# Kernel optimization log

Measured on AMD Instinct MI355X. Metric: run time of the kernel, lower is better.

## Reference

```python
import jax, jax.numpy as jnp
import numpy as np

K = 16
EPS = 1e-5
SLOPE = 0.2


def knn_idx(k, xyz_k, xyz_q):
    # xyz_k: (B,Nk,3), xyz_q: (B,Nq,3) -> (B,Nq,k) indices of k nearest in xyz_k
    d = (jnp.sum(xyz_q * xyz_q, -1, keepdims=True)
         - 2.0 * jnp.einsum('bqc,bkc->bqk', xyz_q, xyz_k)
         + jnp.sum(xyz_k * xyz_k, -1)[:, None, :])
    _, idx = jax.lax.top_k(-d, k)
    return idx


def graph_feature(coor_q, x_q, coor_k, x_k):
    # coor_*: (B,N*,3); x_q: (B,C,Nq); x_k: (B,C,Nk) -> (B,2C,Nq,K)
    idx = knn_idx(K, coor_k, coor_q)                      # (B,Nq,K)
    nbr = jax.vmap(lambda xk, i: xk[:, i])(x_k, idx)       # (B,C,Nq,K)
    xq = x_q[:, :, :, None]                                # (B,C,Nq,1)
    xq = jnp.broadcast_to(xq, nbr.shape)
    return jnp.concatenate([nbr - xq, xq], axis=1)


def group_norm(x, gamma, beta, groups=4):
    B, C, N, Kk = x.shape
    xg = x.reshape(B, groups, C // groups, N, Kk)
    mu = jnp.mean(xg, axis=(2, 3, 4), keepdims=True)
    var = jnp.var(xg, axis=(2, 3, 4), keepdims=True)
    xn = ((xg - mu) / jnp.sqrt(var + EPS)).reshape(B, C, N, Kk)
    return xn * gamma[None, :, None, None] + beta[None, :, None, None]


def cgl(f, W, gamma, beta):
    # 1x1 Conv2d (no bias) + GroupNorm(4) + LeakyReLU(0.2)
    y = jnp.einsum('oc,bcnk->bonk', W, f)
    return jax.nn.leaky_relu(group_norm(y, gamma, beta), SLOPE)


def fps(xyz, m):
    # furthest point sampling. xyz: (B,N,3) -> (B,m) int32
    B, N, _ = xyz.shape
    first = jnp.zeros((B,), jnp.int32)

    def body(carry, _):
        dist, last = carry
        lp = jnp.take_along_axis(xyz, last[:, None, None].astype(jnp.int32), axis=1)  # (B,1,3)
        d = jnp.sum((xyz - lp) ** 2, -1)
        dist = jnp.minimum(dist, d)
        nxt = jnp.argmax(dist, -1).astype(jnp.int32)
        return (dist, nxt), nxt

    init = (jnp.full((B, N), 1e10, jnp.float32), first)
    _, rest = jax.lax.scan(body, init, None, length=m - 1)  # (m-1,B)
    return jnp.concatenate([first[None, :], rest], axis=0).T  # (B,m)


def fps_downsample(coor, x, m):
    # coor: (B,N,3), x: (B,C,N) -> new_coor (B,3,m), new_x (B,C,m)
    idx = fps(coor, m)                                        # (B,m)
    new_coor = jnp.take_along_axis(coor, idx[:, :, None], axis=1).transpose(0, 2, 1)
    new_x = jnp.take_along_axis(x, idx[:, None, :], axis=2)
    return new_coor, new_x


def setup_inputs() -> dict:
    key = jax.random.key(0)
    ks = jax.random.split(key, 16)
    d = {
        'x': jax.random.normal(ks[0], (8, 4096, 3), jnp.float32),
        'num0': 2048, 'num1': 512, 'num2': 128,
        'w_in': jax.random.normal(ks[1], (8, 3), jnp.float32) * 0.3,
        'b_in': jnp.zeros((8,), jnp.float32),
    }
    layer_dims = {'1': (32, 16), '2': (64, 64), '4': (128, 128),
                  '5': (128, 256), '6': (256, 256), '7': (256, 512)}
    for i, (name, (o, c)) in enumerate(layer_dims.items()):
        d[f'w{name}'] = jax.random.normal(ks[2 + i], (o, c), jnp.float32) * (1.0 / np.sqrt(c))
        d[f'g{name}'] = jnp.ones((o,), jnp.float32)
        d[f'be{name}'] = jnp.zeros((o,), jnp.float32)
    return d


def reference(x, num0, num1, num2, w_in, b_in,
              w1, g1, be1, w2, g2, be2, w4, g4, be4,
              w5, g5, be5, w6, g6, be6, w7, g7, be7):
    xyz = x.transpose(0, 2, 1)                                # (B,3,N)
    coor = x                                                  # (B,N,3)
    f = jnp.einsum('oc,bcn->bon', w_in, xyz) + b_in[None, :, None]  # (B,8,N)

    f = cgl(graph_feature(coor, f, coor, f), w1, g1, be1)     # (B,32,N,K)
    f = jnp.max(f, axis=-1)                                   # (B,32,N)

    sp1, f_q = fps_downsample(coor, f, num0)                  # (B,3,n0),(B,32,n0)
    coor_d = sp1.transpose(0, 2, 1)                           # (B,n0,3)
    f = cgl(graph_feature(coor_d, f_q, coor, f), w2, g2, be2)
    stage1_feature = jnp.max(f, axis=-1)                      # (B,64,n0)
    coor = coor_d

    sp2, f_q = fps_downsample(coor, stage1_feature, num1)
    coor_d = sp2.transpose(0, 2, 1)
    f = cgl(graph_feature(coor_d, f_q, coor, stage1_feature), w4, g4, be4)
    f = jnp.max(f, axis=-1)                                   # (B,128,n1)
    f = cgl(graph_feature(coor_d, f, coor_d, f), w5, g5, be5)
    stage2_feature = jnp.max(f, axis=-1)                      # (B,128,n1)
    coor = coor_d

    sp3, f_q = fps_downsample(coor, stage2_feature, num2)
    coor_d = sp3.transpose(0, 2, 1)
    f = cgl(graph_feature(coor_d, f_q, coor, stage2_feature), w6, g6, be6)
    f = jnp.max(f, axis=-1)                                   # (B,256,n2)
    f = cgl(graph_feature(coor_d, f, coor_d, f), w7, g7, be7)
    stage3_feature = jnp.max(f, axis=-1)                      # (B,256,n2)

    out_coor = sp3.transpose(0, 2, 1)                         # (B,n2,3)
    out_f = stage3_feature.transpose(0, 2, 1)                 # (B,n2,256)
    return out_coor, out_f
```

## Files before the change

kernel.cpp:

```cpp
#include <hip/hip_runtime.h>
#include <hip/hip_bf16.h>
#include <math.h>

#define DEVI __device__ __forceinline__
typedef unsigned long long ull;
typedef float f32x2 __attribute__((ext_vector_type(2)));

__global__ void k_feat0(const float* __restrict__ x,
                        const float* __restrict__ w_in,
                        const float* __restrict__ b_in,
                        float* __restrict__ coords0, float* __restrict__ feat0,
                        float* __restrict__ stats)
{
  int t = blockIdx.x*blockDim.x + threadIdx.x;
  if (t < 384) stats[t] = 0.f;
  if (t >= 8*4096) return;
  float cx = x[t*3+0], cy = x[t*3+1], cz = x[t*3+2];
  coords0[t*3+0]=cx; coords0[t*3+1]=cy; coords0[t*3+2]=cz;
  #pragma unroll
  for (int o=0;o<8;o++){
    float s = __fadd_rn(__fadd_rn(__fmul_rn(cx,w_in[o*3+0]),
                                  __fmul_rn(cy,w_in[o*3+1])),
                        __fmul_rn(cz,w_in[o*3+2]));
    feat0[t*8+o] = __fadd_rn(s, b_in[o]);
  }
}

DEVI f32x2 pk_sub(f32x2 a, f32x2 b){
  f32x2 r;
  asm("v_pk_add_f32 %0, %1, %2 neg_lo:[0,1] neg_hi:[0,1]" : "=v"(r) : "v"(a), "v"(b));
  return r;
}
DEVI f32x2 pk_mul(f32x2 a, f32x2 b){
  f32x2 r; asm("v_pk_mul_f32 %0, %1, %2" : "=v"(r) : "v"(a), "v"(b)); return r;
}
DEVI f32x2 pk_add(f32x2 a, f32x2 b){
  f32x2 r; asm("v_pk_add_f32 %0, %1, %2" : "=v"(r) : "v"(a), "v"(b)); return r;
}

template<int CTRL>
DEVI float dppmaxf(float x){
  float o = __int_as_float(__builtin_amdgcn_update_dpp(__float_as_int(x),__float_as_int(x),CTRL,0xF,0xF,false));
  return fmaxf(x,o);
}
template<int CTRL>
DEVI unsigned dppminu(unsigned x){
  unsigned o = (unsigned)__builtin_amdgcn_update_dpp((int)x,(int)x,CTRL,0xF,0xF,false);
  return (x < o) ? x : o;
}

template<int P>
DEVI void fps_stage(f32x2 (&px)[P/2], f32x2 (&py)[P/2], f32x2 (&pz)[P/2],
                    int m, float sx, float sy, float sz,
                    const float* cpx, const float* cpy, const float* cpz,
                    ull* mK,
                    int* ssel, float* snx, float* sny, float* snz, int tid)
{
  const int wv = tid>>6, lane = tid&63;
  float dist[P];
  #pragma unroll
  for (int p=0;p<P;p++) dist[p]=1e10f;
  if (tid==0){ ssel[0]=0; if (snx){ snx[0]=sx; sny[0]=sy; snz[0]=sz; } }
  #pragma unroll 1
  for (int it=1; it<m; it++){
    f32x2 vsx, vsy, vsz;
    vsx.x=sx; vsx.y=sx; vsy.x=sy; vsy.y=sy; vsz.x=sz; vsz.y=sz;
    float bv = -1.f;
    #pragma unroll
    for (int i=0;i<P/2;i++){
      f32x2 dx = pk_sub(px[i], vsx);
      f32x2 dy = pk_sub(py[i], vsy);
      f32x2 dz = pk_sub(pz[i], vsz);
      f32x2 s  = pk_add(pk_add(pk_mul(dx,dx), pk_mul(dy,dy)), pk_mul(dz,dz));
      float d0 = fminf(dist[2*i],   s.x);
      float d1 = fminf(dist[2*i+1], s.y);
      dist[2*i] = d0; dist[2*i+1] = d1;
      bv = fmaxf(bv, d0);
      bv = fmaxf(bv, d1);
    }
    int bidx = 0;
    #pragma unroll
    for (int p=P-1;p>=0;p--) if (dist[p]==bv) bidx = tid+(p<<8);
    float w = bv;
    w = dppmaxf<0x111>(w);
    w = dppmaxf<0x112>(w);
    w = dppmaxf<0x114>(w);
    w = dppmaxf<0x118>(w);
    w = dppmaxf<0x142>(w);
    w = dppmaxf<0x143>(w);
    float bvw = __uint_as_float((unsigned)__builtin_amdgcn_readlane(__float_as_int(w),63));
    unsigned cand = (bv == bvw) ? (unsigned)bidx : 0xFFFFFFFFu;
    cand = dppminu<0x111>(cand);
    cand = dppminu<0x112>(cand);
    cand = dppminu<0x114>(cand);
    cand = dppminu<0x118>(cand);
    cand = dppminu<0x142>(cand);
    cand = dppminu<0x143>(cand);
    const unsigned itu = (unsigned)it;
    ull* slot = mK + ((it&1)<<2);
    if (lane==63){
      unsigned lo = ((~cand & 0xFFFu)<<12) | itu;
      *(volatile ull*)(slot + wv) = ((ull)__float_as_uint(bvw)<<32) | (ull)lo;
    }
    ull k0,k1,k2,k3;
    for (;;){
      asm volatile("" ::: "memory");
      k0=slot[0]; k1=slot[1]; k2=slot[2]; k3=slot[3];
      unsigned chk = (((unsigned)k0 ^ itu) | ((unsigned)k1 ^ itu) |
                      ((unsigned)k2 ^ itu) | ((unsigned)k3 ^ itu)) & 0xFFFu;
      if (chk == 0u) break;
    }
    ull ka = (k1>k0)?k1:k0;
    ull kb = (k3>k2)?k3:k2;
    ull kw = (kb>ka)?kb:ka;
    int gi = (int)((~((unsigned)(kw & 0xffffffffull) >> 12)) & 0xFFFu);
    sx = cpx[gi]; sy = cpy[gi]; sz = cpz[gi];
    if (tid==0){
      ssel[it]=gi;
      if (snx){ snx[it]=sx; sny[it]=sy; snz[it]=sz; }
    }
  }
}

template<int CTRL>
DEVI void dppmin_fj(float& d, int& j){
  float od = __int_as_float(__builtin_amdgcn_update_dpp(__float_as_int(d),__float_as_int(d),CTRL,0xF,0xF,false));
  int   oj = __builtin_amdgcn_update_dpp(j,j,CTRL,0xF,0xF,false);
  bool tk = (od < d) || (od == d && oj < j);
  d = tk?od:d; j = tk?oj:j;
}

DEVI float dist_qk(const float* __restrict__ ckb, int j,
                   float qx, float qy, float qz, float sqq){
  float kx=ckb[3*j], ky=ckb[3*j+1], kz=ckb[3*j+2];
  float sk  = __fadd_rn(__fadd_rn(__fmul_rn(kx,kx),__fmul_rn(ky,ky)),
                        __fmul_rn(kz,kz));
  float dot = __fadd_rn(__fadd_rn(__fmul_rn(qx,kx),__fmul_rn(qy,ky)),
                        __fmul_rn(qz,kz));
  return __fadd_rn(__fsub_rn(sqq, __fmul_rn(2.0f,dot)), sk);
}

template<int NPL>
DEVI void knn_wave(const float* __restrict__ cq, int Nq,
                   const float* __restrict__ ck, int Nk,
                   int* __restrict__ idx_out, int b, int q, int lane)
{
  size_t r3 = ((size_t)b*Nq+q)*3;
  float qx=cq[r3], qy=cq[r3+1], qz=cq[r3+2];
  float sqq = __fadd_rn(__fadd_rn(__fmul_rn(qx,qx),__fmul_rn(qy,qy)),
                        __fmul_rn(qz,qz));
  constexpr int GS = (NPL < 8) ? NPL : 8;
  constexpr int NG = NPL / GS;
  float gv[NG]; int gj[NG];
  const float* ckb = ck + (size_t)b*Nk*3;
  ull exmask = 0;
  int dirtyg = -1;
  int myout = 0;
  #pragma unroll 1
  for (int r=0; r<16; r++){
    #pragma unroll
    for (int g=0; g<NG; g++){
      if (dirtyg < 0 || dirtyg == g){
        float nv=__int_as_float(0x7f800000); int nj=0x7fffffff;
        #pragma unroll
        for (int e=0; e<GS; e++){
          const int i = g*GS+e;
          int j = lane + (i<<6);
          float d = dist_qk(ckb, j, qx,qy,qz, sqq);
          bool rem = ((exmask >> i) & 1ull) == 0ull;
          if (rem && d < nv){ nv=d; nj=j; }
        }
        gv[g]=nv; gj[g]=nj;
      }
    }
    float lv = gv[0]; int lj = gj[0];
    #pragma unroll
    for (int g=1; g<NG; g++)
      if (gv[g]<lv || (gv[g]==lv && gj[g]<lj)){ lv=gv[g]; lj=gj[g]; }
    float rd = lv; int rj = lj;
    dppmin_fj<0x111>(rd,rj);
    dppmin_fj<0x112>(rd,rj);
    dppmin_fj<0x114>(rd,rj);
    dppmin_fj<0x118>(rd,rj);
    dppmin_fj<0x142>(rd,rj);
    dppmin_fj<0x143>(rd,rj);
    int wj = __builtin_amdgcn_readlane(rj,63);
    if (lane == r) myout = wj;
    if ((wj & 63) == lane) exmask |= (1ull << (wj>>6));
    dirtyg = (wj>>6)/GS;
  }
  if (lane<16) idx_out[((size_t)b*Nq+q)*16 + lane] = myout;
}

__global__ __launch_bounds__(256) void k_fps_knn1(
    const float* __restrict__ coords0,
    int* __restrict__ idx1, int* __restrict__ idx2, int* __restrict__ idx3,
    float* __restrict__ c1, float* __restrict__ c2, float* __restrict__ c3,
    float* __restrict__ out, int* __restrict__ knn1)
{
  __shared__ float s1x[4096], s1y[4096], s1z[4096];
  __shared__ float s2x[2048], s2y[2048], s2z[2048];
  __shared__ float s3x[512],  s3y[512],  s3z[512];
  __shared__ float s4x[128],  s4y[128],  s4z[128];
  __shared__ int   ssel[2048];
  __shared__ alignas(32) ull mK[8];
  if (blockIdx.x >= 8){
    int flat = blockIdx.x - 8;
    int b = flat >> 10, qb = flat & 1023;
    int q = qb*4 + (threadIdx.x>>6);
    knn_wave<64>(coords0, 4096, coords0, 4096, knn1, b, q, threadIdx.x&63);
    return;
  }
  const int b = blockIdx.x, tid = threadIdx.x;
  __builtin_amdgcn_s_setprio(3);
  const float* cb = coords0 + (size_t)b*4096*3;
  if (tid<8) mK[tid] = ~0ull;
  {
    f32x2 px[8], py[8], pz[8];
    #pragma unroll
    for (int i=0;i<8;i++){
      int j0 = tid + ((2*i)<<8), j1 = tid + ((2*i+1)<<8);
      float X0=cb[3*j0], Y0=cb[3*j0+1], Z0=cb[3*j0+2];
      float X1=cb[3*j1], Y1=cb[3*j1+1], Z1=cb[3*j1+2];
      px[i].x=X0; px[i].y=X1; py[i].x=Y0; py[i].y=Y1; pz[i].x=Z0; pz[i].y=Z1;
      s1x[j0]=X0; s1y[j0]=Y0; s1z[j0]=Z0;
      s1x[j1]=X1; s1y[j1]=Y1; s1z[j1]=Z1;
    }
    float sx=cb[0], sy=cb[1], sz=cb[2];
    __syncthreads();
    fps_stage<16>(px,py,pz, 2048, sx,sy,sz, s1x,s1y,s1z,
                  mK, ssel, s2x,s2y,s2z, tid);
  }
  __syncthreads();
  {
    float* c1b = c1 + (size_t)b*2048*3;
    for (int i=tid;i<2048;i+=256){
      idx1[b*2048+i]=ssel[i];
      c1b[3*i]=s2x[i]; c1b[3*i+1]=s2y[i]; c1b[3*i+2]=s2z[i];
    }
  }
  {
    f32x2 px[4], py[4], pz[4];
    #pragma unroll
    for (int i=0;i<4;i++){
      int j0 = tid + ((2*i)<<8), j1 = tid + ((2*i+1)<<8);
      px[i].x=s2x[j0]; px[i].y=s2x[j1];
      py[i].x=s2y[j0]; py[i].y=s2y[j1];
      pz[i].x=s2z[j0]; pz[i].y=s2z[j1];
    }
    float sx=s2x[0], sy=s2y[0], sz=s2z[0];
    __syncthreads();
    fps_stage<8>(px,py,pz, 512, sx,sy,sz, s2x,s2y,s2z,
                 mK, ssel, s3x,s3y,s3z, tid);
  }
  __syncthreads();
  {
    float* c2b = c2 + (size_t)b*512*3;
    for (int i=tid;i<512;i+=256){
      idx2[b*512+i]=ssel[i];
      c2b[3*i]=s3x[i]; c2b[3*i+1]=s3y[i]; c2b[3*i+2]=s3z[i];
    }
  }
  {
    f32x2 px[1], py[1], pz[1];
    {
      int j0 = tid, j1 = tid + 256;
      px[0].x=s3x[j0]; px[0].y=s3x[j1];
      py[0].x=s3y[j0]; py[0].y=s3y[j1];
      pz[0].x=s3z[j0]; pz[0].y=s3z[j1];
    }
    float sx=s3x[0], sy=s3y[0], sz=s3z[0];
    __syncthreads();
    fps_stage<2>(px,py,pz, 128, sx,sy,sz, s3x,s3y,s3z,
                 mK, ssel, s4x,s4y,s4z, tid);
  }
  __syncthreads();
  {
    float* c3b = c3 + (size_t)b*128*3;
    float* ob  = out + (size_t)b*128*3;
    for (int i=tid;i<128;i+=256){
      idx3[b*128+i]=ssel[i];
      float X=s4x[i],Y=s4y[i],Z=s4z[i];
      c3b[3*i]=X; c3b[3*i+1]=Y; c3b[3*i+2]=Z;
      ob[3*i]=X; ob[3*i+1]=Y; ob[3*i+2]=Z;
    }
  }
}

struct WtParams {
  const float* W[6];
  float* wl[6];
  float* wq[6];
  int O[6], C[6], OC[6];
};
__global__ void k_wt_all(WtParams p){
  int s = blockIdx.y;
  int t = blockIdx.x*blockDim.x + threadIdx.x;
  int OC = p.OC[s];
  if (t >= OC) return;
  int C = p.C[s], O = p.O[s];
  int o = t / C, c = t - o*C;
  const float* W = p.W[s];
  float wlv = W[o*2*C + c];
  float wrv = W[o*2*C + C + c];
  p.wl[s][c*O+o] = wlv;
  p.wq[s][c*O+o] = wrv - wlv;
}

#define GEMM_M 8
template<int NPL>
__global__ __launch_bounds__(256,3) void k_knn_gemm(
    const float* __restrict__ cq, int Nq,
    const float* __restrict__ ck, int Nk, int* __restrict__ knnidx,
    const float* __restrict__ feat, int C, int O,
    const float* __restrict__ wlT, const float* __restrict__ wqT,
    float* __restrict__ yk, float* __restrict__ yq, int gknn)
{
  const int b = blockIdx.y;
  if ((int)blockIdx.x < gknn){
    int q = blockIdx.x*4 + (threadIdx.x>>6);
    if (q < Nq) knn_wave<NPL>(cq, Nq, ck, Nk, knnidx, b, q, threadIdx.x&63);
    return;
  }
  const int bx = blockIdx.x - gknn;
  extern __shared__ float sf[];
  const int o = threadIdx.x & (O-1);
  const int rg = threadIdx.x / O;
  const int R = blockDim.x / O;
  const int rowsPB = R*GEMM_M;
  const int row0 = bx * rowsPB;
  const int Cp = C+1;
  const float* src = feat + ((size_t)b*Nk + row0)*C;
  for (int i=threadIdx.x; i<rowsPB*C; i+=blockDim.x){
    int r = i / C, c = i - r*C;
    sf[r*Cp + c] = src[i];
  }
  __syncthreads();
  float ak[GEMM_M], aq[GEMM_M];
  #pragma unroll
  for (int m=0;m<GEMM_M;m++){ ak[m]=0.f; aq[m]=0.f; }
  const float* lp = wlT + o;
  const float* qp = wqT + o;
  const float* sfr = sf + rg*GEMM_M*Cp;
  for (int c=0;c<C;c++){
    float wl = lp[(size_t)c*O];
    float wq = qp[(size_t)c*O];
    #pragma unroll
    for (int m=0;m<GEMM_M;m++){
      float xv = sfr[m*Cp + c];
      ak[m] = fmaf(xv, wl, ak[m]);
      aq[m] = fmaf(xv, wq, aq[m]);
    }
  }
  size_t obase = ((size_t)b*Nk + row0 + rg*GEMM_M)*O + o;
  #pragma unroll
  for (int m=0;m<GEMM_M;m++){
    yk[obase + (size_t)m*O] = ak[m];
    yq[obase + (size_t)m*O] = aq[m];
  }
}

__global__ void k_gather(const float* __restrict__ yk, const float* __restrict__ yq,
                         const int* __restrict__ knnidx, const int* __restrict__ qmap,
                         int Nq, int Nk, int O,
                         float* __restrict__ vmax, float* __restrict__ stats)
{
  const int b = blockIdx.y;
  const int o = threadIdx.x & (O-1);
  const int rg = threadIdx.x / O;
  const int R = blockDim.x / O;
  float ls=0.f, ls2=0.f;
  const float* ykb = yk + (size_t)b*Nk*O;
  const float* yqb = yq + (size_t)b*Nk*O;
  for (int nq = blockIdx.x*R + rg; nq < Nq; nq += gridDim.x*R){
    int qj = qmap ? qmap[b*Nq+nq] : nq;
    float vq = yqb[(size_t)qj*O + o];
    const int* ip = knnidx + ((size_t)b*Nq+nq)*16;
    float vmx = -3.4e38f;
    #pragma unroll
    for (int k=0;k<16;k++){
      int j = ip[k];
      float v = ykb[(size_t)j*O+o] + vq;
      vmx = fmaxf(vmx, v);
      ls += v; ls2 = fmaf(v,v,ls2);
    }
    vmax[((size_t)b*Nq+nq)*O+o] = vmx;
  }
  int span = O/4; if (span>64) span=64;
  for (int mm=1; mm<span; mm<<=1){
    ls  += __shfl_xor(ls, mm);
    ls2 += __shfl_xor(ls2, mm);
  }
  __shared__ float sred[8];
  if (threadIdx.x<8) sred[threadIdx.x]=0.f;
  __syncthreads();
  int lane = threadIdx.x & 63;
  if ((lane & (span-1))==0){
    int g = (o*4)/O;
    atomicAdd(&sred[g*2+0], ls);
    atomicAdd(&sred[g*2+1], ls2);
  }
  __syncthreads();
  if (threadIdx.x<8) atomicAdd(&stats[b*8+threadIdx.x], sred[threadIdx.x]);
}

__global__ void k_norm(const float* __restrict__ vmax, const float* __restrict__ stats,
                       const float* __restrict__ gamma,
                       const float* __restrict__ beta,
                       int Nq, int O, float invcnt, float* __restrict__ outf)
{
  const int b = blockIdx.y;
  const int n = Nq*O;
  for (int i = blockIdx.x*blockDim.x+threadIdx.x; i<n; i+=gridDim.x*blockDim.x){
    int o = i & (O-1);
    int g = (o*4)/O;
    float s1 = stats[b*8+g*2], s2 = stats[b*8+g*2+1];
    float mu = s1*invcnt;
    float var = fmaf(-mu,mu, s2*invcnt);
    float rs = 1.0f/sqrtf(var+1e-5f);
    float v = (vmax[(size_t)b*n + i]-mu)*rs*gamma[o] + beta[o];
    outf[(size_t)b*n + i] = (v>=0.f)? v : 0.2f*v;
  }
}

extern "C" void kernel_launch(void* const* d_in, const int* in_sizes, int n_in,
                              void* d_out, int out_size, void* d_ws, size_t ws_size,
                              hipStream_t stream)
{
  const int B = 8;
  const float* x    = (const float*)d_in[0];
  const float* w_in = (const float*)d_in[4];
  const float* b_in = (const float*)d_in[5];
  const float *Wm[6], *Gm[6], *Bm[6];
  for (int i=0;i<6;i++){
    Wm[i]=(const float*)d_in[6+3*i];
    Gm[i]=(const float*)d_in[6+3*i+1];
    Bm[i]=(const float*)d_in[6+3*i+2];
  }
  float* ws = (float*)d_ws;
  float* out = (float*)d_out;
  const size_t OFF_C0=0,        OFF_F0=98304,   OFF_F1=360448,  OFF_F2=1409024,
               OFF_F4=2457600,  OFF_F5=2981888, OFF_F6=3506176, OFF_F7=3768320,
               OFF_C1=4030464,  OFF_C2=4079616, OFF_C3=4091904,
               OFF_YK=4094976,  OFF_YQ=6192128, OFF_VM=8289280,
               OFF_WL=9337856,  OFF_WQ=9468928, OFF_ST=9600000,
               OFF_I1=9600384,  OFF_I2=9616768, OFF_I3=9620864, OFF_KNN=9621888,
               TOTAL=10146176;
  if (ws_size < TOTAL*sizeof(float)) return;
  float *c0=ws+OFF_C0, *f0=ws+OFF_F0, *f1=ws+OFF_F1, *f2=ws+OFF_F2,
        *f4=ws+OFF_F4, *f5=ws+OFF_F5, *f6=ws+OFF_F6,
        *c1=ws+OFF_C1, *c2=ws+OFF_C2, *c3=ws+OFF_C3,
        *yk=ws+OFF_YK, *yq=ws+OFF_YQ, *vm=ws+OFF_VM, *stats=ws+OFF_ST;
  int *i1=(int*)(ws+OFF_I1), *i2=(int*)(ws+OFF_I2), *i3=(int*)(ws+OFF_I3),
      *knn=(int*)(ws+OFF_KNN);

  const int OCs[6]  = {256, 2048, 8192, 16384, 32768, 65536};
  const int OCoff[6]= {0,   256,  2304, 10496, 26880, 59648};

  struct St { int C,O,Nk,Nq; const float* feat; const float* cq; const float* ck;
              const int* qmap; float* outf; };
  const St st[6] = {
    {8,   32, 4096, 4096, f0, c0, c0, nullptr, f1},
    {32,  64, 4096, 2048, f1, c1, c0, i1,      f2},
    {64, 128, 2048,  512, f2, c2, c1, i2,      f4},
    {128,128,  512,  512, f4, c2, c2, nullptr, f5},
    {128,256,  512,  128, f5, c3, c2, i3,      f6},
    {256,256,  128,  128, f6, c3, c3, nullptr, out + 8*128*3},
  };

  k_feat0 <<<(8*4096+255)/256, 256, 0, stream>>>(x, w_in, b_in, c0, f0, stats);

  WtParams wp;
  for (int s=0;s<6;s++){
    wp.W[s]=Wm[s];
    wp.wl[s]=ws+OFF_WL+OCoff[s];
    wp.wq[s]=ws+OFF_WQ+OCoff[s];
    wp.O[s]=st[s].O; wp.C[s]=st[s].C; wp.OC[s]=OCs[s];
  }
  k_wt_all<<<dim3(256,6), 256, 0, stream>>>(wp);

  k_fps_knn1<<<8 + 8*1024, 256, 0, stream>>>(c0, i1, i2, i3, c1, c2, c3,
                                             out, knn);

  for (int s=0;s<6;s++){
    const St& S = st[s];
    int rowsPB = 2048 / S.O;
    int ggemm = S.Nk / rowsPB;
    int gknn  = (s > 0) ? (S.Nq + 3)/4 : 0;
    dim3 gg(gknn + ggemm, B);
    size_t shb = (size_t)rowsPB * (S.C+1) * sizeof(float);
    int npl = S.Nk >> 6;
    if      (s == 0)    k_knn_gemm< 2><<<gg, 256, shb, stream>>>(S.cq,S.Nq,S.ck,S.Nk,knn,
                                   S.feat,S.C,S.O, ws+OFF_WL+OCoff[s], ws+OFF_WQ+OCoff[s],
                                   yk, yq, gknn);
    else if (npl == 64) k_knn_gemm<64><<<gg, 256, shb, stream>>>(S.cq,S.Nq,S.ck,S.Nk,knn,
                                   S.feat,S.C,S.O, ws+OFF_WL+OCoff[s], ws+OFF_WQ+OCoff[s],
                                   yk, yq, gknn);
    else if (npl == 32) k_knn_gemm<32><<<gg, 256, shb, stream>>>(S.cq,S.Nq,S.ck,S.Nk,knn,
                                   S.feat,S.C,S.O, ws+OFF_WL+OCoff[s], ws+OFF_WQ+OCoff[s],
                                   yk, yq, gknn);
    else if (npl ==  8) k_knn_gemm< 8><<<gg, 256, shb, stream>>>(S.cq,S.Nq,S.ck,S.Nk,knn,
                                   S.feat,S.C,S.O, ws+OFF_WL+OCoff[s], ws+OFF_WQ+OCoff[s],
                                   yk, yq, gknn);
    else                k_knn_gemm< 2><<<gg, 256, shb, stream>>>(S.cq,S.Nq,S.ck,S.Nk,knn,
                                   S.feat,S.C,S.O, ws+OFF_WL+OCoff[s], ws+OFF_WQ+OCoff[s],
                                   yk, yq, gknn);
    dim3 gs(64, B);
    k_gather<<<gs, 256, 0, stream>>>(yk, yq, knn, S.qmap, S.Nq, S.Nk, S.O,
                                     vm, stats + s*64);
    float invcnt = 1.0f / ((float)(S.O/4) * (float)S.Nq * 16.0f);
    dim3 gn((S.Nq*S.O + 255)/256, B);
    k_norm<<<gn, 256, 0, stream>>>(vm, stats + s*64, Gm[s], Bm[s],
                                   S.Nq, S.O, invcnt, S.outf);
  }
}
```

Measured before the change: 2.300 ms.

## Fuse GroupNorm+LeakyReLU and input projection into next stage GEMM load

Removes the separate k_feat0 kernel by computing the input linear projection while the stage-0 GEMM loads its tile, and drops per-stage k_norm launches by applying the previous stage's group norm and LeakyReLU as tiles are loaded into shared memory. Only the final stage still runs k_norm to write the output. Stats zeroing moves into the weight-transpose kernel, and the raw input is used directly as coordinates. This saves kernel launches and intermediate round-trips, at the cost of recomputing the normalisation per element during each load.

New measurement: 2.293 ms. About the same (-0.3%).

```diff
diff --git a/kernel.cpp b/kernel.cpp
--- a/kernel.cpp
+++ b/kernel.cpp
@@ -5,26 +5,6 @@
 #define DEVI __device__ __forceinline__
 typedef unsigned long long ull;
 typedef float f32x2 __attribute__((ext_vector_type(2)));
-
-__global__ void k_feat0(const float* __restrict__ x,
-                        const float* __restrict__ w_in,
-                        const float* __restrict__ b_in,
-                        float* __restrict__ coords0, float* __restrict__ feat0,
-                        float* __restrict__ stats)
-{
-  int t = blockIdx.x*blockDim.x + threadIdx.x;
-  if (t < 384) stats[t] = 0.f;
-  if (t >= 8*4096) return;
-  float cx = x[t*3+0], cy = x[t*3+1], cz = x[t*3+2];
-  coords0[t*3+0]=cx; coords0[t*3+1]=cy; coords0[t*3+2]=cz;
-  #pragma unroll
-  for (int o=0;o<8;o++){
-    float s = __fadd_rn(__fadd_rn(__fmul_rn(cx,w_in[o*3+0]),
-                                  __fmul_rn(cy,w_in[o*3+1])),
-                        __fmul_rn(cz,w_in[o*3+2]));
-    feat0[t*8+o] = __fadd_rn(s, b_in[o]);
-  }
-}
 
 DEVI f32x2 pk_sub(f32x2 a, f32x2 b){
   f32x2 r;
@@ -293,9 +273,10 @@
   float* wq[6];
   int O[6], C[6], OC[6];
 };
-__global__ void k_wt_all(WtParams p){
+__global__ void k_wt_all(WtParams p, float* __restrict__ stats){
   int s = blockIdx.y;
   int t = blockIdx.x*blockDim.x + threadIdx.x;
+  if (s==0 && t<384) stats[t] = 0.f;
   int OC = p.OC[s];
   if (t >= OC) return;
   int C = p.C[s], O = p.O[s];
@@ -308,11 +289,15 @@
 }
 
 #define GEMM_M 8
-template<int NPL>
+template<int NPL, int MODE>
 __global__ __launch_bounds__(256,3) void k_knn_gemm(
     const float* __restrict__ cq, int Nq,
     const float* __restrict__ ck, int Nk, int* __restrict__ knnidx,
-    const float* __restrict__ feat, int C, int O,
+    const float* __restrict__ fsrc,
+    const float* __restrict__ w_in, const float* __restrict__ b_in,
+    const float* __restrict__ stats, const float* __restrict__ gamma,
+    const float* __restrict__ beta, float invcnt,
+    int C, int O,
     const float* __restrict__ wlT, const float* __restrict__ wqT,
     float* __restrict__ yk, float* __restrict__ yq, int gknn)
 {
@@ -330,10 +315,29 @@
   const int rowsPB = R*GEMM_M;
   const int row0 = bx * rowsPB;
   const int Cp = C+1;
-  const float* src = feat + ((size_t)b*Nk + row0)*C;
-  for (int i=threadIdx.x; i<rowsPB*C; i+=blockDim.x){
-    int r = i / C, c = i - r*C;
-    sf[r*Cp + c] = src[i];
+  if (MODE == 0){
+    const float* xb = fsrc + (size_t)b*Nk*3;
+    for (int i=threadIdx.x; i<rowsPB*C; i+=blockDim.x){
+      int r = i / C, c = i - r*C;
+      int row = row0 + r;
+      float cx=xb[row*3], cy=xb[row*3+1], cz=xb[row*3+2];
+      float s = __fadd_rn(__fadd_rn(__fmul_rn(cx,w_in[c*3+0]),
+                                    __fmul_rn(cy,w_in[c*3+1])),
+                          __fmul_rn(cz,w_in[c*3+2]));
+      sf[r*Cp + c] = __fadd_rn(s, b_in[c]);
+    }
+  } else {
+    const float* src = fsrc + ((size_t)b*Nk + row0)*C;
+    for (int i=threadIdx.x; i<rowsPB*C; i+=blockDim.x){
+      int r = i / C, c = i - r*C;
+      int g = (c*4)/C;
+      float s1 = stats[b*8+g*2], s2 = stats[b*8+g*2+1];
+      float mu = s1*invcnt;
+      float var = fmaf(-mu,mu, s2*invcnt);
+      float rs = 1.0f/sqrtf(var+1e-5f);
+      float v = (src[i]-mu)*rs*gamma[c] + beta[c];
+      sf[r*Cp + c] = (v>=0.f)? v : 0.2f*v;
+    }
   }
   __syncthreads();
   float ak[GEMM_M], aq[GEMM_M];
@@ -447,28 +451,29 @@
                OFF_I1=9600384,  OFF_I2=9616768, OFF_I3=9620864, OFF_KNN=9621888,
                TOTAL=10146176;
   if (ws_size < TOTAL*sizeof(float)) return;
-  float *c0=ws+OFF_C0, *f0=ws+OFF_F0, *f1=ws+OFF_F1, *f2=ws+OFF_F2,
-        *f4=ws+OFF_F4, *f5=ws+OFF_F5, *f6=ws+OFF_F6,
-        *c1=ws+OFF_C1, *c2=ws+OFF_C2, *c3=ws+OFF_C3,
+  float *c1=ws+OFF_C1, *c2=ws+OFF_C2, *c3=ws+OFF_C3,
         *yk=ws+OFF_YK, *yq=ws+OFF_YQ, *vm=ws+OFF_VM, *stats=ws+OFF_ST;
   int *i1=(int*)(ws+OFF_I1), *i2=(int*)(ws+OFF_I2), *i3=(int*)(ws+OFF_I3),
       *knn=(int*)(ws+OFF_KNN);
+  (void)OFF_C0; (void)OFF_F0; (void)OFF_F1; (void)OFF_F2; (void)OFF_F4;
+  (void)OFF_F5; (void)OFF_F6; (void)OFF_F7;
 
   const int OCs[6]  = {256, 2048, 8192, 16384, 32768, 65536};
   const int OCoff[6]= {0,   256,  2304, 10496, 26880, 59648};
 
-  struct St { int C,O,Nk,Nq; const float* feat; const float* cq; const float* ck;
-              const int* qmap; float* outf; };
+  struct St { int C,O,Nk,Nq; const float* cq; const float* ck;
+              const int* qmap; };
   const St st[6] = {
-    {8,   32, 4096, 4096, f0, c0, c0, nullptr, f1},
-    {32,  64, 4096, 2048, f1, c1, c0, i1,      f2},
-    {64, 128, 2048,  512, f2, c2, c1, i2,      f4},
-    {128,128,  512,  512, f4, c2, c2, nullptr, f5},
-    {128,256,  512,  128, f5, c3, c2, i3,      f6},
-    {256,256,  128,  128, f6, c3, c3, nullptr, out + 8*128*3},
+    {8,   32, 4096, 4096, x,  x,  nullptr},
+    {32,  64, 4096, 2048, c1, x,  i1},
+    {64, 128, 2048,  512, c2, c1, i2},
+    {128,128,  512,  512, c2, c2, nullptr},
+    {128,256,  512,  128, c3, c2, i3},
+    {256,256,  128,  128, c3, c3, nullptr},
   };
-
-  k_feat0 <<<(8*4096+255)/256, 256, 0, stream>>>(x, w_in, b_in, c0, f0, stats);
+  float invc[6];
+  for (int s=0;s<6;s++)
+    invc[s] = 1.0f / ((float)(st[s].O/4) * (float)st[s].Nq * 16.0f);
 
   WtParams wp;
   for (int s=0;s<6;s++){
@@ -477,9 +482,9 @@
     wp.wq[s]=ws+OFF_WQ+OCoff[s];
     wp.O[s]=st[s].O; wp.C[s]=st[s].C; wp.OC[s]=OCs[s];
   }
-  k_wt_all<<<dim3(256,6), 256, 0, stream>>>(wp);
-
-  k_fps_knn1<<<8 + 8*1024, 256, 0, stream>>>(c0, i1, i2, i3, c1, c2, c3,
+  k_wt_all<<<dim3(256,6), 256, 0, stream>>>(wp, stats);
+
+  k_fps_knn1<<<8 + 8*1024, 256, 0, stream>>>(x, i1, i2, i3, c1, c2, c3,
                                              out, knn);
 
   for (int s=0;s<6;s++){
@@ -489,28 +494,40 @@
     int gknn  = (s > 0) ? (S.Nq + 3)/4 : 0;
     dim3 gg(gknn + ggemm, B);
     size_t shb = (size_t)rowsPB * (S.C+1) * sizeof(float);
+    const float* wl = ws+OFF_WL+OCoff[s];
+    const float* wqp = ws+OFF_WQ+OCoff[s];
+    const float* stp = (s>0) ? (stats + (s-1)*64) : nullptr;
+    const float* gp  = (s>0) ? Gm[s-1] : nullptr;
+    const float* bp  = (s>0) ? Bm[s-1] : nullptr;
+    float ivc = (s>0) ? invc[s-1] : 0.f;
     int npl = S.Nk >> 6;
-    if      (s == 0)    k_knn_gemm< 2><<<gg, 256, shb, stream>>>(S.cq,S.Nq,S.ck,S.Nk,knn,
-                                   S.feat,S.C,S.O, ws+OFF_WL+OCoff[s], ws+OFF_WQ+OCoff[s],
-                                   yk, yq, gknn);
-    else if (npl == 64) k_knn_gemm<64><<<gg, 256, shb, stream>>>(S.cq,S.Nq,S.ck,S.Nk,knn,
-                                   S.feat,S.C,S.O, ws+OFF_WL+OCoff[s], ws+OFF_WQ+OCoff[s],
-                                   yk, yq, gknn);
-    else if (npl == 32) k_knn_gemm<32><<<gg, 256, shb, stream>>>(S.cq,S.Nq,S.ck,S.Nk,knn,
-                                   S.feat,S.C,S.O, ws+OFF_WL+OCoff[s], ws+OFF_WQ+OCoff[s],
-                                   yk, yq, gknn);
-    else if (npl ==  8) k_knn_gemm< 8><<<gg, 256, shb, stream>>>(S.cq,S.Nq,S.ck,S.Nk,knn,
-                                   S.feat,S.C,S.O, ws+OFF_WL+OCoff[s], ws+OFF_WQ+OCoff[s],
-                                   yk, yq, gknn);
-    else                k_knn_gemm< 2><<<gg, 256, shb, stream>>>(S.cq,S.Nq,S.ck,S.Nk,knn,
-                                   S.feat,S.C,S.O, ws+OFF_WL+OCoff[s], ws+OFF_WQ+OCoff[s],
-                                   yk, yq, gknn);
+    if      (s == 0)
+      k_knn_gemm< 2,0><<<gg, 256, shb, stream>>>(S.cq,S.Nq,S.ck,S.Nk,knn,
+        x, w_in, b_in, nullptr, nullptr, nullptr, 0.f,
+        S.C, S.O, wl, wqp, yk, yq, gknn);
+    else if (npl == 64)
+      k_knn_gemm<64,1><<<gg, 256, shb, stream>>>(S.cq,S.Nq,S.ck,S.Nk,knn,
+        vm, nullptr, nullptr, stp, gp, bp, ivc,
+        S.C, S.O, wl, wqp, yk, yq, gknn);
+    else if (npl == 32)
+      k_knn_gemm<32,1><<<gg, 256, shb, stream>>>(S.cq,S.Nq,S.ck,S.Nk,knn,
+        vm, nullptr, nullptr, stp, gp, bp, ivc,
+        S.C, S.O, wl, wqp, yk, yq, gknn);
+    else if (npl ==  8)
+      k_knn_gemm< 8,1><<<gg, 256, shb, stream>>>(S.cq,S.Nq,S.ck,S.Nk,knn,
+        vm, nullptr, nullptr, stp, gp, bp, ivc,
+        S.C, S.O, wl, wqp, yk, yq, gknn);
+    else
+      k_knn_gemm< 2,1><<<gg, 256, shb, stream>>>(S.cq,S.Nq,S.ck,S.Nk,knn,
+        vm, nullptr, nullptr, stp, gp, bp, ivc,
+        S.C, S.O, wl, wqp, yk, yq, gknn);
     dim3 gs(64, B);
     k_gather<<<gs, 256, 0, stream>>>(yk, yq, knn, S.qmap, S.Nq, S.Nk, S.O,
                                      vm, stats + s*64);
-    float invcnt = 1.0f / ((float)(S.O/4) * (float)S.Nq * 16.0f);
-    dim3 gn((S.Nq*S.O + 255)/256, B);
-    k_norm<<<gn, 256, 0, stream>>>(vm, stats + s*64, Gm[s], Bm[s],
-                                   S.Nq, S.O, invcnt, S.outf);
-  }
-}
+  }
+  {
+    dim3 gn((128*256 + 255)/256, B);
+    k_norm<<<gn, 256, 0, stream>>>(vm, stats + 5*64, Gm[5], Bm[5],
+                                   128, 256, invc[5], out + 8*128*3);
+  }
+}
```
